# Kernel optimization log

Hardware: AMD Instinct MI355X
Metric: run time of the kernel (lower is better)

Reference implementation:

```python
import jax, jax.numpy as jnp
import numpy as np

N = 8192
IN_F = 256
OUT_F = 64
ALPHA = 0.2  # LeakyReLU negative slope
NEG_INF = -9e15


def setup_inputs() -> dict:
    key = jax.random.key(0)
    k1, k2, k3, k4 = jax.random.split(key, 4)
    input_h = jax.random.normal(k1, (N, IN_F), dtype=jnp.float32)
    # xavier_normal with gain=1.414 ~ std = 1.414*sqrt(2/(fan_in+fan_out))
    W = jax.random.normal(k2, (IN_F, OUT_F), dtype=jnp.float32) * (1.414 * np.sqrt(2.0 / (IN_F + OUT_F)))
    a = jax.random.normal(k3, (2 * OUT_F, 1), dtype=jnp.float32) * (1.414 * np.sqrt(2.0 / (2 * OUT_F + 1)))
    adj = jax.random.randint(k4, (N, N), 0, 2).astype(jnp.int32)
    return {"input_h": input_h, "adj": adj, "W": W, "a": a}


def reference(input_h, adj, W, a):
    # h = X @ W : [N, OUT_F]
    h = input_h @ W
    # Pairwise concat score: a^T [h_i || h_j] == (h_i @ a1) + (h_j @ a2)
    a1 = a[:OUT_F]   # [OUT_F, 1]
    a2 = a[OUT_F:]   # [OUT_F, 1]
    f1 = h @ a1      # [N, 1] -> contribution of source node i
    f2 = h @ a2      # [N, 1] -> contribution of target node j
    e = jax.nn.leaky_relu(f1 + f2.T, negative_slope=ALPHA)  # [N, N]
    # Masked softmax over neighbors (adj > 0), dropout is identity in eval mode
    attention = jax.nn.softmax(jnp.where(adj > 0, e, NEG_INF), axis=-1)
    h_prime = attention @ h  # [N, OUT_F]
    # concat=True -> ELU activation
    return jax.nn.elu(h_prime)
```

## Files before the change

kernel.cpp:

```cpp
#include <hip/hip_runtime.h>
#include <hip/hip_bf16.h>


using short8 = __attribute__((ext_vector_type(8))) short;
using f32x4  = __attribute__((ext_vector_type(4))) float;

#define NN     8192
#define INF_   256
#define OUTF   64
#define LR_A   0.2f
#define ROWS   16
#define TILE_C 256
#define NTILES (NN / TILE_C)
#define ROWB   1040

__device__ __forceinline__ unsigned short f2bf_rne(float x) {
  unsigned int u = __float_as_uint(x);
  u += 0x7FFFu + ((u >> 16) & 1u);
  return (unsigned short)(u >> 16);
}

__global__ __launch_bounds__(256) void gat_pre(
    const float* __restrict__ input, const float* __restrict__ W,
    const float* __restrict__ a, unsigned short* __restrict__ hp,
    float* __restrict__ f1, float* __restrict__ f2) {
  __shared__ float WT[OUTF][260];
  int tid = threadIdx.x;
  for (int idx = tid; idx < INF_ * OUTF; idx += 256) {
    int c = idx >> 6, f = idx & 63;
    WT[f][c] = W[idx];
  }
  __syncthreads();
  int w = tid >> 6, l = tid & 63;
  int i0 = blockIdx.x * 16 + w * 4;
  const float4* r0 = (const float4*)(input + (long)(i0 + 0) * INF_);
  const float4* r1 = (const float4*)(input + (long)(i0 + 1) * INF_);
  const float4* r2 = (const float4*)(input + (long)(i0 + 2) * INF_);
  const float4* r3 = (const float4*)(input + (long)(i0 + 3) * INF_);
  float h0 = 0.f, h1 = 0.f, h2 = 0.f, h3 = 0.f;
#pragma unroll 4
  for (int c4 = 0; c4 < INF_ / 4; ++c4) {
    float4 wv = *(const float4*)&WT[l][c4 * 4];
    float4 v0 = r0[c4], v1 = r1[c4], v2 = r2[c4], v3 = r3[c4];
    h0 = fmaf(v0.x, wv.x, h0); h0 = fmaf(v0.y, wv.y, h0);
    h0 = fmaf(v0.z, wv.z, h0); h0 = fmaf(v0.w, wv.w, h0);
    h1 = fmaf(v1.x, wv.x, h1); h1 = fmaf(v1.y, wv.y, h1);
    h1 = fmaf(v1.z, wv.z, h1); h1 = fmaf(v1.w, wv.w, h1);
    h2 = fmaf(v2.x, wv.x, h2); h2 = fmaf(v2.y, wv.y, h2);
    h2 = fmaf(v2.z, wv.z, h2); h2 = fmaf(v2.w, wv.w, h2);
    h3 = fmaf(v3.x, wv.x, h3); h3 = fmaf(v3.y, wv.y, h3);
    h3 = fmaf(v3.z, wv.z, h3); h3 = fmaf(v3.w, wv.w, h3);
  }
  float a1k = a[l], a2k = a[OUTF + l];
  float hh[4] = {h0, h1, h2, h3};
#pragma unroll
  for (int r = 0; r < 4; ++r) {
    int i = i0 + r;
    float t1 = hh[r] * a1k, t2 = hh[r] * a2k;
#pragma unroll
    for (int off = 32; off; off >>= 1) {
      t1 += __shfl_xor(t1, off);
      t2 += __shfl_xor(t2, off);
    }
    int gran = (((i >> 5) * 4) + (l >> 4)) * 64 + ((i >> 3) & 3) * 16 + (l & 15);
    hp[(long)gran * 8 + (i & 7)] = f2bf_rne(hh[r]);
    if (l == 0) { f1[i] = t1; f2[i] = t2; }
  }
}

__global__ __launch_bounds__(512, 4) void gat_main(
    const int* __restrict__ adj, const unsigned short* __restrict__ hp,
    const float* __restrict__ f1, const float* __restrict__ f2,
    float* __restrict__ out) {
  __shared__ __align__(16) char um[2 * ROWS * ROWB];
  __shared__ float ssum[8][ROWS];
  __shared__ float f1s[ROWS], shifts[ROWS], red[8];
  int tid = threadIdx.x;
  int w = tid >> 6, l = tid & 63;
  int i0 = blockIdx.x * ROWS;

  float fm = -1e30f;
  for (int jj = tid; jj < NN; jj += 512) fm = fmaxf(fm, f2[jj]);
#pragma unroll
  for (int off = 32; off; off >>= 1) fm = fmaxf(fm, __shfl_xor(fm, off));
  if (l == 0) red[w] = fm;
  __syncthreads();
  if (tid == 0) {
    float m = red[0];
#pragma unroll
    for (int x = 1; x < 8; ++x) m = fmaxf(m, red[x]);
    red[0] = m;
  }
  __syncthreads();
  float Fmax = red[0];
  if (tid < ROWS) {
    float v = f1[i0 + tid];
    f1s[tid] = v;
    float s = v + Fmax;
    shifts[tid] = fmaxf(s, LR_A * s);
  }
  __syncthreads();

  int q = l & 15, g = l >> 4;
  float f1r = f1s[q], sh = shifts[q];
  float u1 = f1r - sh;
  float u2 = LR_A * f1r - sh;
  f32x4 acc0 = {0.f, 0.f, 0.f, 0.f}, acc1 = acc0, acc2 = acc0, acc3 = acc0;
  float srow = 0.f;

  auto stage = [&](int t, int b) {
    const int* src0 = adj + (long)(i0 + 2 * w) * NN + t * TILE_C + l * 4;
    const int* src1 = src0 + NN;
    char* d0 = um + b * (ROWS * ROWB) + (2 * w) * ROWB;
    char* d1 = d0 + ROWB;
    __builtin_amdgcn_global_load_lds(
        (const __attribute__((address_space(1))) void*)src0,
        (__attribute__((address_space(3))) void*)d0, 16, 0, 0);
    __builtin_amdgcn_global_load_lds(
        (const __attribute__((address_space(1))) void*)src1,
        (__attribute__((address_space(3))) void*)d1, 16, 0, 0);
  };

  stage(0, 0);
  __syncthreads();

  for (int t = 0; t < NTILES; ++t) {
    int b = t & 1;
    if (t + 1 < NTILES) stage(t + 1, b ^ 1);

    const char* base = um + b * (ROWS * ROWB) + q * ROWB + w * 128 + g * 32;
    int4 A0 = *(const int4*)(base);
    int4 A1 = *(const int4*)(base + 16);
    int jb = t * TILE_C + w * 32 + g * 8;
    float4 F0 = *(const float4*)(f2 + jb);
    float4 F1 = *(const float4*)(f2 + jb + 4);
    float fa[8] = {F0.x, F0.y, F0.z, F0.w, F1.x, F1.y, F1.z, F1.w};
    int   aa[8] = {A0.x, A0.y, A0.z, A0.w, A1.x, A1.y, A1.z, A1.w};

    union { short8 v; unsigned short u[8]; } pa;
    float ps = 0.f;
#pragma unroll
    for (int e = 0; e < 8; ++e) {
      float arg = fmaxf(u1 + fa[e], fmaf(LR_A, fa[e], u2));
      float pe = (aa[e] > 0) ? __expf(arg) : 0.f;
      ps += pe;
      pa.u[e] = f2bf_rne(pe);
    }
    srow += ps;

    long gb = ((long)(t * 8 + w) * 4) * 64 * 8;
    short8 b0 = *(const short8*)(hp + gb + (0 * 64 + l) * 8);
    short8 b1 = *(const short8*)(hp + gb + (1 * 64 + l) * 8);
    short8 b2 = *(const short8*)(hp + gb + (2 * 64 + l) * 8);
    short8 b3 = *(const short8*)(hp + gb + (3 * 64 + l) * 8);
    acc0 = __builtin_amdgcn_mfma_f32_16x16x32_bf16(pa.v, b0, acc0, 0, 0, 0);
    acc1 = __builtin_amdgcn_mfma_f32_16x16x32_bf16(pa.v, b1, acc1, 0, 0, 0);
    acc2 = __builtin_amdgcn_mfma_f32_16x16x32_bf16(pa.v, b2, acc2, 0, 0, 0);
    acc3 = __builtin_amdgcn_mfma_f32_16x16x32_bf16(pa.v, b3, acc3, 0, 0, 0);

    __syncthreads();
  }

  srow += __shfl_xor(srow, 16);
  srow += __shfl_xor(srow, 32);
  if (l < ROWS) ssum[w][l] = srow;

  float* accs = (float*)um;
#pragma unroll
  for (int r = 0; r < 4; ++r) {
    accs[(w * ROWS + g * 4 + r) * OUTF + 0 * 16 + q] = acc0[r];
    accs[(w * ROWS + g * 4 + r) * OUTF + 1 * 16 + q] = acc1[r];
    accs[(w * ROWS + g * 4 + r) * OUTF + 2 * 16 + q] = acc2[r];
    accs[(w * ROWS + g * 4 + r) * OUTF + 3 * 16 + q] = acc3[r];
  }
  __syncthreads();

  for (int idx = tid; idx < ROWS * OUTF; idx += 512) {
    int m = idx >> 6, n = idx & 63;
    float num = 0.f, den = 0.f;
#pragma unroll
    for (int ww = 0; ww < 8; ++ww) {
      num += accs[(ww * ROWS + m) * OUTF + n];
      den += ssum[ww][m];
    }
    float v = num / den;
    out[(long)(i0 + m) * OUTF + n] = v > 0.f ? v : expm1f(v);
  }
}

extern "C" void kernel_launch(void* const* d_in, const int* in_sizes, int n_in,
                              void* d_out, int out_size, void* d_ws, size_t ws_size,
                              hipStream_t stream) {
  const float* input = (const float*)d_in[0];
  const int*   adj   = (const int*)d_in[1];
  const float* W     = (const float*)d_in[2];
  const float* a     = (const float*)d_in[3];
  float* out = (float*)d_out;
  char* ws = (char*)d_ws;
  unsigned short* hp = (unsigned short*)ws;
  float* f1 = (float*)(ws + (1 << 20));
  float* f2 = (float*)(ws + (1 << 20) + (32 << 10));
  (void)in_sizes; (void)n_in; (void)out_size; (void)ws_size;

  gat_pre<<<512, 256, 0, stream>>>(input, W, a, hp, f1, f2);
  gat_main<<<512, 512, 0, stream>>>(adj, hp, f1, f2, out);
}
```

Baseline: 101.5 us.

## Split neighbor columns across four blocks per row tile with separate reduction kernel

The main attention kernel now splits the 8192 neighbor columns into four chunks handled by separate 256-thread blocks (grid 512x4), giving four times as many blocks so more CUs stay busy and more adjacency loads are in flight. Each block writes partial numerators and denominators to workspace, and a new finalize kernel sums the four partials, divides, and applies ELU. The logits are pre-scaled by log2(e) so exp2f can replace __expf. The cost is an extra kernel launch and about 8 MB of partial-sum write and read traffic.

```diff
diff --git a/kernel.cpp b/kernel.cpp
--- a/kernel.cpp
+++ b/kernel.cpp
@@ -9,9 +9,11 @@
 #define INF_   256
 #define OUTF   64
 #define LR_A   0.2f
+#define LOG2E  1.4426950408889634f
 #define ROWS   16
 #define TILE_C 256
-#define NTILES (NN / TILE_C)
+#define CQW    2048
+#define NTILES (CQW / TILE_C)
 #define ROWB   1040
 
 __device__ __forceinline__ unsigned short f2bf_rne(float x) {
@@ -64,31 +66,33 @@
     }
     int gran = (((i >> 5) * 4) + (l >> 4)) * 64 + ((i >> 3) & 3) * 16 + (l & 15);
     hp[(long)gran * 8 + (i & 7)] = f2bf_rne(hh[r]);
-    if (l == 0) { f1[i] = t1; f2[i] = t2; }
-  }
-}
-
-__global__ __launch_bounds__(512, 4) void gat_main(
+    if (l == 0) { f1[i] = t1 * LOG2E; f2[i] = t2 * LOG2E; }
+  }
+}
+
+__global__ __launch_bounds__(256, 4) void gat_main(
     const int* __restrict__ adj, const unsigned short* __restrict__ hp,
     const float* __restrict__ f1, const float* __restrict__ f2,
-    float* __restrict__ out) {
+    float* __restrict__ numP, float* __restrict__ denP) {
   __shared__ __align__(16) char um[2 * ROWS * ROWB];
-  __shared__ float ssum[8][ROWS];
-  __shared__ float f1s[ROWS], shifts[ROWS], red[8];
+  __shared__ float ssum[4][ROWS];
+  __shared__ float f1s[ROWS], shifts[ROWS], red[4];
   int tid = threadIdx.x;
   int w = tid >> 6, l = tid & 63;
   int i0 = blockIdx.x * ROWS;
+  int cq = blockIdx.y;
 
   float fm = -1e30f;
-  for (int jj = tid; jj < NN; jj += 512) fm = fmaxf(fm, f2[jj]);
+  for (int jj = tid * 4; jj < NN; jj += 256 * 4) {
+    float4 v = *(const float4*)(f2 + jj);
+    fm = fmaxf(fm, fmaxf(fmaxf(v.x, v.y), fmaxf(v.z, v.w)));
+  }
 #pragma unroll
   for (int off = 32; off; off >>= 1) fm = fmaxf(fm, __shfl_xor(fm, off));
   if (l == 0) red[w] = fm;
   __syncthreads();
   if (tid == 0) {
-    float m = red[0];
-#pragma unroll
-    for (int x = 1; x < 8; ++x) m = fmaxf(m, red[x]);
+    float m = fmaxf(fmaxf(red[0], red[1]), fmaxf(red[2], red[3]));
     red[0] = m;
   }
   __syncthreads();
@@ -108,17 +112,18 @@
   f32x4 acc0 = {0.f, 0.f, 0.f, 0.f}, acc1 = acc0, acc2 = acc0, acc3 = acc0;
   float srow = 0.f;
 
+  const int* adjb = adj + (long)cq * CQW;
+
   auto stage = [&](int t, int b) {
-    const int* src0 = adj + (long)(i0 + 2 * w) * NN + t * TILE_C + l * 4;
-    const int* src1 = src0 + NN;
-    char* d0 = um + b * (ROWS * ROWB) + (2 * w) * ROWB;
-    char* d1 = d0 + ROWB;
-    __builtin_amdgcn_global_load_lds(
-        (const __attribute__((address_space(1))) void*)src0,
-        (__attribute__((address_space(3))) void*)d0, 16, 0, 0);
-    __builtin_amdgcn_global_load_lds(
-        (const __attribute__((address_space(1))) void*)src1,
-        (__attribute__((address_space(3))) void*)d1, 16, 0, 0);
+#pragma unroll
+    for (int k = 0; k < 4; ++k) {
+      int r = w * 4 + k;
+      const int* src = adjb + (long)(i0 + r) * NN + t * TILE_C + l * 4;
+      char* d = um + b * (ROWS * ROWB) + r * ROWB;
+      __builtin_amdgcn_global_load_lds(
+          (const __attribute__((address_space(1))) void*)src,
+          (__attribute__((address_space(3))) void*)d, 16, 0, 0);
+    }
   };
 
   stage(0, 0);
@@ -128,36 +133,40 @@
     int b = t & 1;
     if (t + 1 < NTILES) stage(t + 1, b ^ 1);
 
-    const char* base = um + b * (ROWS * ROWB) + q * ROWB + w * 128 + g * 32;
-    int4 A0 = *(const int4*)(base);
-    int4 A1 = *(const int4*)(base + 16);
-    int jb = t * TILE_C + w * 32 + g * 8;
-    float4 F0 = *(const float4*)(f2 + jb);
-    float4 F1 = *(const float4*)(f2 + jb + 4);
-    float fa[8] = {F0.x, F0.y, F0.z, F0.w, F1.x, F1.y, F1.z, F1.w};
-    int   aa[8] = {A0.x, A0.y, A0.z, A0.w, A1.x, A1.y, A1.z, A1.w};
-
-    union { short8 v; unsigned short u[8]; } pa;
-    float ps = 0.f;
-#pragma unroll
-    for (int e = 0; e < 8; ++e) {
-      float arg = fmaxf(u1 + fa[e], fmaf(LR_A, fa[e], u2));
-      float pe = (aa[e] > 0) ? __expf(arg) : 0.f;
-      ps += pe;
-      pa.u[e] = f2bf_rne(pe);
-    }
-    srow += ps;
-
-    long gb = ((long)(t * 8 + w) * 4) * 64 * 8;
-    short8 b0 = *(const short8*)(hp + gb + (0 * 64 + l) * 8);
-    short8 b1 = *(const short8*)(hp + gb + (1 * 64 + l) * 8);
-    short8 b2 = *(const short8*)(hp + gb + (2 * 64 + l) * 8);
-    short8 b3 = *(const short8*)(hp + gb + (3 * 64 + l) * 8);
-    acc0 = __builtin_amdgcn_mfma_f32_16x16x32_bf16(pa.v, b0, acc0, 0, 0, 0);
-    acc1 = __builtin_amdgcn_mfma_f32_16x16x32_bf16(pa.v, b1, acc1, 0, 0, 0);
-    acc2 = __builtin_amdgcn_mfma_f32_16x16x32_bf16(pa.v, b2, acc2, 0, 0, 0);
-    acc3 = __builtin_amdgcn_mfma_f32_16x16x32_bf16(pa.v, b3, acc3, 0, 0, 0);
-
+    const char* base = um + b * (ROWS * ROWB) + q * ROWB;
+#pragma unroll
+    for (int s = 0; s < 2; ++s) {
+      int koff = w * 256 + s * 128 + g * 32;
+      int4 A0 = *(const int4*)(base + koff);
+      int4 A1 = *(const int4*)(base + koff + 16);
+      int jb = cq * CQW + t * TILE_C + w * 64 + s * 32 + g * 8;
+      float4 F0 = *(const float4*)(f2 + jb);
+      float4 F1 = *(const float4*)(f2 + jb + 4);
+      float fa[8] = {F0.x, F0.y, F0.z, F0.w, F1.x, F1.y, F1.z, F1.w};
+      int   aa[8] = {A0.x, A0.y, A0.z, A0.w, A1.x, A1.y, A1.z, A1.w};
+
+      union { short8 v; unsigned short u[8]; } pa;
+      float ps = 0.f;
+#pragma unroll
+      for (int e = 0; e < 8; ++e) {
+        float arg = fmaxf(u1 + fa[e], fmaf(LR_A, fa[e], u2));
+        float pe = (aa[e] > 0) ? exp2f(arg) : 0.f;
+        ps += pe;
+        pa.u[e] = f2bf_rne(pe);
+      }
+      srow += ps;
+
+      int K32 = cq * 64 + t * 8 + w * 2 + s;
+      const unsigned short* hb = hp + (long)K32 * 4 * 64 * 8 + l * 8;
+      short8 b0 = *(const short8*)(hb + 0 * 64 * 8);
+      short8 b1 = *(const short8*)(hb + 1 * 64 * 8);
+      short8 b2 = *(const short8*)(hb + 2 * 64 * 8);
+      short8 b3 = *(const short8*)(hb + 3 * 64 * 8);
+      acc0 = __builtin_amdgcn_mfma_f32_16x16x32_bf16(pa.v, b0, acc0, 0, 0, 0);
+      acc1 = __builtin_amdgcn_mfma_f32_16x16x32_bf16(pa.v, b1, acc1, 0, 0, 0);
+      acc2 = __builtin_amdgcn_mfma_f32_16x16x32_bf16(pa.v, b2, acc2, 0, 0, 0);
+      acc3 = __builtin_amdgcn_mfma_f32_16x16x32_bf16(pa.v, b3, acc3, 0, 0, 0);
+    }
     __syncthreads();
   }
 
@@ -175,17 +184,32 @@
   }
   __syncthreads();
 
-  for (int idx = tid; idx < ROWS * OUTF; idx += 512) {
+  for (int idx = tid; idx < ROWS * OUTF; idx += 256) {
     int m = idx >> 6, n = idx & 63;
     float num = 0.f, den = 0.f;
 #pragma unroll
-    for (int ww = 0; ww < 8; ++ww) {
+    for (int ww = 0; ww < 4; ++ww) {
       num += accs[(ww * ROWS + m) * OUTF + n];
       den += ssum[ww][m];
     }
-    float v = num / den;
-    out[(long)(i0 + m) * OUTF + n] = v > 0.f ? v : expm1f(v);
-  }
+    numP[((long)cq * NN + i0 + m) * OUTF + n] = num;
+    if (n == 0) denP[(long)cq * NN + i0 + m] = den;
+  }
+}
+
+__global__ __launch_bounds__(256) void gat_fin(
+    const float* __restrict__ numP, const float* __restrict__ denP,
+    float* __restrict__ out) {
+  int gid = blockIdx.x * 256 + threadIdx.x;
+  int row = gid >> 6, n = gid & 63;
+  float num = 0.f, den = 0.f;
+#pragma unroll
+  for (int c = 0; c < 4; ++c) {
+    num += numP[((long)c * NN + row) * OUTF + n];
+    den += denP[(long)c * NN + row];
+  }
+  float v = num / den;
+  out[gid] = v > 0.f ? v : expm1f(v);
 }
 
 extern "C" void kernel_launch(void* const* d_in, const int* in_sizes, int n_in,
@@ -198,10 +222,13 @@
   float* out = (float*)d_out;
   char* ws = (char*)d_ws;
   unsigned short* hp = (unsigned short*)ws;
-  float* f1 = (float*)(ws + (1 << 20));
-  float* f2 = (float*)(ws + (1 << 20) + (32 << 10));
+  float* f1   = (float*)(ws + (1 << 20));
+  float* f2   = (float*)(ws + (1 << 20) + (32 << 10));
+  float* numP = (float*)(ws + (1 << 20) + (64 << 10));
+  float* denP = (float*)(ws + (1 << 20) + (64 << 10) + (8 << 20));
   (void)in_sizes; (void)n_in; (void)out_size; (void)ws_size;
 
   gat_pre<<<512, 256, 0, stream>>>(input, W, a, hp, f1, f2);
-  gat_main<<<512, 512, 0, stream>>>(adj, hp, f1, f2, out);
-}
+  gat_main<<<dim3(512, 4), 256, 0, stream>>>(adj, hp, f1, f2, numP, denP);
+  gat_fin<<<NN * OUTF / 256, 256, 0, stream>>>(numP, denP, out);
+}
```

New measurement: 100.2 us. Within noise of the previous version (-1.3%).

## Prepack adjacency rows into LDS bitmasks and drop per-tile block barriers

Applied to the files above, without the earlier changes.

The main kernel now runs 256-thread blocks. It streams each block's 16 adjacency rows once up front and packs them into an LDS bitmask, and it also caches the whole f2 vector in LDS. The inner loop then runs with no __syncthreads, double-buffering the bf16 h fragments in registers, and it uses exp2f on log2e-prescaled scores instead of __expf. This removes the per-tile block barrier and the staged int32 adjacency loads. The cost is a serialized upfront adjacency read that no longer overlaps compute, plus about 49KB of LDS per block, which limits occupancy.

```diff
diff --git a/kernel.cpp b/kernel.cpp
--- a/kernel.cpp
+++ b/kernel.cpp
@@ -9,10 +9,9 @@
 #define INF_   256
 #define OUTF   64
 #define LR_A   0.2f
+#define LOG2E  1.4426950408889634f
 #define ROWS   16
-#define TILE_C 256
-#define NTILES (NN / TILE_C)
-#define ROWB   1040
+#define BPAD   1040
 
 __device__ __forceinline__ unsigned short f2bf_rne(float x) {
   unsigned int u = __float_as_uint(x);
@@ -64,33 +63,33 @@
     }
     int gran = (((i >> 5) * 4) + (l >> 4)) * 64 + ((i >> 3) & 3) * 16 + (l & 15);
     hp[(long)gran * 8 + (i & 7)] = f2bf_rne(hh[r]);
-    if (l == 0) { f1[i] = t1; f2[i] = t2; }
-  }
-}
-
-__global__ __launch_bounds__(512, 4) void gat_main(
+    if (l == 0) { f1[i] = t1 * LOG2E; f2[i] = t2 * LOG2E; }
+  }
+}
+
+__global__ __launch_bounds__(256, 3) void gat_main(
     const int* __restrict__ adj, const unsigned short* __restrict__ hp,
     const float* __restrict__ f1, const float* __restrict__ f2,
     float* __restrict__ out) {
-  __shared__ __align__(16) char um[2 * ROWS * ROWB];
-  __shared__ float ssum[8][ROWS];
-  __shared__ float f1s[ROWS], shifts[ROWS], red[8];
+  __shared__ __align__(16) unsigned char bitsL[ROWS * BPAD];
+  __shared__ float f2s[NN];
+  __shared__ float ssum[4][ROWS];
+  __shared__ float f1s[ROWS], shifts[ROWS], red[4];
   int tid = threadIdx.x;
   int w = tid >> 6, l = tid & 63;
   int i0 = blockIdx.x * ROWS;
 
   float fm = -1e30f;
-  for (int jj = tid; jj < NN; jj += 512) fm = fmaxf(fm, f2[jj]);
+  for (int jj = tid * 4; jj < NN; jj += 1024) {
+    float4 v = *(const float4*)(f2 + jj);
+    *(float4*)&f2s[jj] = v;
+    fm = fmaxf(fm, fmaxf(fmaxf(v.x, v.y), fmaxf(v.z, v.w)));
+  }
 #pragma unroll
   for (int off = 32; off; off >>= 1) fm = fmaxf(fm, __shfl_xor(fm, off));
   if (l == 0) red[w] = fm;
   __syncthreads();
-  if (tid == 0) {
-    float m = red[0];
-#pragma unroll
-    for (int x = 1; x < 8; ++x) m = fmaxf(m, red[x]);
-    red[0] = m;
-  }
+  if (tid == 0) red[0] = fmaxf(fmaxf(red[0], red[1]), fmaxf(red[2], red[3]));
   __syncthreads();
   float Fmax = red[0];
   if (tid < ROWS) {
@@ -99,73 +98,76 @@
     float s = v + Fmax;
     shifts[tid] = fmaxf(s, LR_A * s);
   }
+
+#pragma unroll
+  for (int r = 0; r < 4; ++r) {
+    int rr = w * 4 + r;
+    const int4* rowp = (const int4*)(adj + (long)(i0 + rr) * NN) + l * 2;
+    unsigned char* brow = bitsL + rr * BPAD + l;
+#pragma unroll 4
+    for (int c = 0; c < 16; ++c) {
+      int4 a = rowp[c * 128], b = rowp[c * 128 + 1];
+      unsigned bt = (a.x > 0) | ((a.y > 0) << 1) | ((a.z > 0) << 2) |
+                    ((a.w > 0) << 3) | ((b.x > 0) << 4) | ((b.y > 0) << 5) |
+                    ((b.z > 0) << 6) | ((b.w > 0) << 7);
+      brow[c * 64] = (unsigned char)bt;
+    }
+  }
   __syncthreads();
 
   int q = l & 15, g = l >> 4;
   float f1r = f1s[q], sh = shifts[q];
-  float u1 = f1r - sh;
-  float u2 = LR_A * f1r - sh;
+  float u1 = f1r - sh, u2 = LR_A * f1r - sh;
   f32x4 acc0 = {0.f, 0.f, 0.f, 0.f}, acc1 = acc0, acc2 = acc0, acc3 = acc0;
   float srow = 0.f;
 
-  auto stage = [&](int t, int b) {
-    const int* src0 = adj + (long)(i0 + 2 * w) * NN + t * TILE_C + l * 4;
-    const int* src1 = src0 + NN;
-    char* d0 = um + b * (ROWS * ROWB) + (2 * w) * ROWB;
-    char* d1 = d0 + ROWB;
-    __builtin_amdgcn_global_load_lds(
-        (const __attribute__((address_space(1))) void*)src0,
-        (__attribute__((address_space(3))) void*)d0, 16, 0, 0);
-    __builtin_amdgcn_global_load_lds(
-        (const __attribute__((address_space(1))) void*)src1,
-        (__attribute__((address_space(3))) void*)d1, 16, 0, 0);
+  const unsigned char* bq = bitsL + q * BPAD + w * 256 + g;
+  const float* f2w = f2s + w * 2048 + g * 8;
+  const unsigned short* hpw = hp + (long)w * 64 * 2048 + l * 8;
+
+  short8 hA[4], hB[4];
+  auto load_hp = [&](short8* d, int t) {
+    const unsigned short* p = hpw + (long)t * 2048;
+    d[0] = *(const short8*)(p);
+    d[1] = *(const short8*)(p + 512);
+    d[2] = *(const short8*)(p + 1024);
+    d[3] = *(const short8*)(p + 1536);
   };
-
-  stage(0, 0);
-  __syncthreads();
-
-  for (int t = 0; t < NTILES; ++t) {
-    int b = t & 1;
-    if (t + 1 < NTILES) stage(t + 1, b ^ 1);
-
-    const char* base = um + b * (ROWS * ROWB) + q * ROWB + w * 128 + g * 32;
-    int4 A0 = *(const int4*)(base);
-    int4 A1 = *(const int4*)(base + 16);
-    int jb = t * TILE_C + w * 32 + g * 8;
-    float4 F0 = *(const float4*)(f2 + jb);
-    float4 F1 = *(const float4*)(f2 + jb + 4);
+  auto compute = [&](int t, const short8* H) {
+    unsigned bt = bq[t * 4];
+    const float* fb = f2w + t * 32;
+    float4 F0 = *(const float4*)fb, F1 = *(const float4*)(fb + 4);
     float fa[8] = {F0.x, F0.y, F0.z, F0.w, F1.x, F1.y, F1.z, F1.w};
-    int   aa[8] = {A0.x, A0.y, A0.z, A0.w, A1.x, A1.y, A1.z, A1.w};
-
     union { short8 v; unsigned short u[8]; } pa;
     float ps = 0.f;
 #pragma unroll
     for (int e = 0; e < 8; ++e) {
       float arg = fmaxf(u1 + fa[e], fmaf(LR_A, fa[e], u2));
-      float pe = (aa[e] > 0) ? __expf(arg) : 0.f;
+      float pe = (bt & (1u << e)) ? exp2f(arg) : 0.f;
       ps += pe;
       pa.u[e] = f2bf_rne(pe);
     }
     srow += ps;
-
-    long gb = ((long)(t * 8 + w) * 4) * 64 * 8;
-    short8 b0 = *(const short8*)(hp + gb + (0 * 64 + l) * 8);
-    short8 b1 = *(const short8*)(hp + gb + (1 * 64 + l) * 8);
-    short8 b2 = *(const short8*)(hp + gb + (2 * 64 + l) * 8);
-    short8 b3 = *(const short8*)(hp + gb + (3 * 64 + l) * 8);
-    acc0 = __builtin_amdgcn_mfma_f32_16x16x32_bf16(pa.v, b0, acc0, 0, 0, 0);
-    acc1 = __builtin_amdgcn_mfma_f32_16x16x32_bf16(pa.v, b1, acc1, 0, 0, 0);
-    acc2 = __builtin_amdgcn_mfma_f32_16x16x32_bf16(pa.v, b2, acc2, 0, 0, 0);
-    acc3 = __builtin_amdgcn_mfma_f32_16x16x32_bf16(pa.v, b3, acc3, 0, 0, 0);
-
-    __syncthreads();
+    acc0 = __builtin_amdgcn_mfma_f32_16x16x32_bf16(pa.v, H[0], acc0, 0, 0, 0);
+    acc1 = __builtin_amdgcn_mfma_f32_16x16x32_bf16(pa.v, H[1], acc1, 0, 0, 0);
+    acc2 = __builtin_amdgcn_mfma_f32_16x16x32_bf16(pa.v, H[2], acc2, 0, 0, 0);
+    acc3 = __builtin_amdgcn_mfma_f32_16x16x32_bf16(pa.v, H[3], acc3, 0, 0, 0);
+  };
+
+  load_hp(hA, 0);
+  for (int tt = 0; tt < 64; tt += 2) {
+    load_hp(hB, tt + 1);
+    compute(tt, hA);
+    if (tt + 2 < 64) load_hp(hA, tt + 2);
+    compute(tt + 1, hB);
   }
 
   srow += __shfl_xor(srow, 16);
   srow += __shfl_xor(srow, 32);
+
+  __syncthreads();
   if (l < ROWS) ssum[w][l] = srow;
-
-  float* accs = (float*)um;
+  float* accs = (float*)bitsL;
 #pragma unroll
   for (int r = 0; r < 4; ++r) {
     accs[(w * ROWS + g * 4 + r) * OUTF + 0 * 16 + q] = acc0[r];
@@ -175,11 +177,11 @@
   }
   __syncthreads();
 
-  for (int idx = tid; idx < ROWS * OUTF; idx += 512) {
+  for (int idx = tid; idx < ROWS * OUTF; idx += 256) {
     int m = idx >> 6, n = idx & 63;
     float num = 0.f, den = 0.f;
 #pragma unroll
-    for (int ww = 0; ww < 8; ++ww) {
+    for (int ww = 0; ww < 4; ++ww) {
       num += accs[(ww * ROWS + m) * OUTF + n];
       den += ssum[ww][m];
     }
@@ -203,5 +205,5 @@
   (void)in_sizes; (void)n_in; (void)out_size; (void)ws_size;
 
   gat_pre<<<512, 256, 0, stream>>>(input, W, a, hp, f1, f2);
-  gat_main<<<512, 512, 0, stream>>>(adj, hp, f1, f2, out);
-}
+  gat_main<<<512, 256, 0, stream>>>(adj, hp, f1, f2, out);
+}
```

After: 106.4 us, median of 2. +4.8%, slower.
